# Kernel optimization log

Measured on AMD Instinct MI355X. Metric: run time of the kernel, lower is better.

The kernel has to match this reference:

```python
import jax, jax.numpy as jnp
import numpy as np

B, S, D_MODEL, NUM_HEADS, MAX_LEN = 4, 1024, 1024, 16, 1024
D_HEAD = D_MODEL // NUM_HEADS


def _skew(QEr):
    # QEr: (b, h, s, s). Music-Transformer skew: pad one col on the left,
    # reshape swapping the last two dims, drop the first row.
    b, h, r, c = QEr.shape
    padded = jnp.pad(QEr, ((0, 0), (0, 0), (0, 0), (1, 0)))  # (b,h,r,c+1)
    reshaped = padded.reshape(b, h, c + 1, r)
    return reshaped[:, :, 1:, :]  # (b,h,s,s)


def setup_inputs() -> dict:
    key = jax.random.key(0)
    ks = jax.random.split(key, 8)
    sc = 1.0 / np.sqrt(D_MODEL).astype(np.float32)
    return {
        "x": jax.random.normal(ks[0], (B, S, D_MODEL), jnp.float32),
        "Wq": jax.random.normal(ks[1], (D_MODEL, D_MODEL), jnp.float32) * sc,
        "bq": jnp.zeros((D_MODEL,), jnp.float32),
        "Wk": jax.random.normal(ks[2], (D_MODEL, D_MODEL), jnp.float32) * sc,
        "bk": jnp.zeros((D_MODEL,), jnp.float32),
        "Wv": jax.random.normal(ks[3], (D_MODEL, D_MODEL), jnp.float32) * sc,
        "bv": jnp.zeros((D_MODEL,), jnp.float32),
        "Er": jax.random.normal(ks[4], (MAX_LEN, D_HEAD), jnp.float32),
    }


def reference(x, Wq, bq, Wk, bk, Wv, bv, Er):
    b, s, _ = x.shape
    h, dh = NUM_HEADS, D_HEAD
    # projections -> (b, h, s, dh). Weights stored [in, out] (equiv. to torch W.T).
    q = (x @ Wq + bq).reshape(b, s, h, dh).transpose(0, 2, 1, 3)
    k = (x @ Wk + bk).reshape(b, s, h, dh).transpose(0, 2, 1, 3)
    v = (x @ Wv + bv).reshape(b, s, h, dh).transpose(0, 2, 1, 3)
    Er_t = Er[MAX_LEN - s:, :]                      # (s, dh)
    QEr = jnp.einsum('bhsd,td->bhst', q, Er_t)      # (b,h,s,s)
    Srel = _skew(QEr)
    scores = (jnp.einsum('bhsd,bhtd->bhst', q, k) + Srel) / np.float32(np.sqrt(dh))
    causal = jnp.tril(jnp.ones((s, s), bool))       # (s,s)
    scores = jnp.where(causal[None, None], scores, -jnp.inf)
    attn = jax.nn.softmax(scores, axis=-1)
    out = jnp.einsum('bhst,bhtd->bhsd', attn, v)    # (b,h,s,dh)
    return out.transpose(0, 2, 1, 3).reshape(b, s, h * dh)
```

## Files before the change

kernel.cpp:

```cpp
#include <hip/hip_runtime.h>
#include <hip/hip_bf16.h>
#include <math.h>

typedef __attribute__((ext_vector_type(8))) short short8;
typedef __attribute__((ext_vector_type(4))) float f32x4;
typedef __attribute__((ext_vector_type(4))) unsigned short us4;
typedef __attribute__((ext_vector_type(2))) unsigned int u32x2;

#define DM 1024
#define NH 16
#define DH 64
#define SS 1024
#define C2 0.180336879f

#define GLDS16(g, l) __builtin_amdgcn_global_load_lds(                      \
    (const __attribute__((address_space(1))) unsigned int*)(g),             \
    (__attribute__((address_space(3))) unsigned int*)(l), 16, 0, 0)

__device__ __forceinline__ unsigned short f2b(float f){
    unsigned int u = __float_as_uint(f);
    u += 0x7fffu + ((u >> 16) & 1u);
    return (unsigned short)(u >> 16);
}
__device__ __forceinline__ float b2f(unsigned short b){
    return __uint_as_float(((unsigned int)b) << 16);
}
__device__ __forceinline__ unsigned int cvt_pk_bf16(float lo, float hi){
    unsigned int r;
    asm volatile("v_cvt_pk_bf16_f32 %0, %1, %2" : "=v"(r) : "v"(lo), "v"(hi));
    return r;
}

__global__ __launch_bounds__(256) void cast_f32_bf16_k(const float* __restrict__ in,
                                                       unsigned short* __restrict__ out){
    int i = (blockIdx.x * 256 + threadIdx.x) * 4;
    float4 v = *(const float4*)(in + i);
    us4 o = { f2b(v.x), f2b(v.y), f2b(v.z), f2b(v.w) };
    *(us4*)(out + i) = o;
}

__global__ __launch_bounds__(256) void transpose_cast_w_k(const float* __restrict__ Wq,
                                                          const float* __restrict__ Wk,
                                                          const float* __restrict__ Wv,
                                                          unsigned short* __restrict__ wT){
    __shared__ float tile[32][33];
    const float* W = blockIdx.z==0 ? Wq : (blockIdx.z==1 ? Wk : Wv);
    int o0 = blockIdx.x*32, k0 = blockIdx.y*32;
    int tx = threadIdx.x, ty = threadIdx.y;
    #pragma unroll
    for (int i=0;i<32;i+=8) tile[ty+i][tx] = W[(k0+ty+i)*DM + o0+tx];
    __syncthreads();
    #pragma unroll
    for (int i=0;i<32;i+=8) wT[(blockIdx.z*DM + o0+ty+i)*DM + k0+tx] = f2b(tile[tx][ty+i]);
}

__global__ __launch_bounds__(256) void gemm_qkv_k(
    const unsigned short* __restrict__ xb, const unsigned short* __restrict__ wT,
    const float* __restrict__ bq, const float* __restrict__ bk, const float* __restrict__ bv,
    unsigned short* __restrict__ Qb, unsigned short* __restrict__ Kb, unsigned short* __restrict__ VTb)
{
    __shared__ unsigned short lda[128*32];
    __shared__ unsigned short ldb[128*32];
    const int tid = threadIdx.x;
    const int lane = tid & 63, w = tid >> 6;
    const int wr = w >> 1, wc = w & 1;
    const int lr = lane & 15, lk = (lane >> 4) * 8, lk4 = lane >> 4;
    const int m0 = blockIdx.y * 128, n0 = blockIdx.x * 128;
    const bool vblk = (n0 >= 2048);
    f32x4 acc[4][4] = {};
    for (int k0 = 0; k0 < DM; k0 += 32){
        #pragma unroll
        for (int p=0;p<2;p++){
            int idx = tid + p*256;
            int row = idx >> 2, cc = (idx & 3) * 8;
            GLDS16(&xb[(m0+row)*DM + k0 + cc], &lda[idx<<3]);
            GLDS16(&wT[(n0+row)*DM + k0 + cc], &ldb[idx<<3]);
        }
        __syncthreads();
        short8 a[4], b[4];
        #pragma unroll
        for (int m=0;m<4;m++) a[m] = *(const short8*)(&lda[(wr*64+m*16+lr)*32 + lk]);
        #pragma unroll
        for (int n=0;n<4;n++) b[n] = *(const short8*)(&ldb[(wc*64+n*16+lr)*32 + lk]);
        __builtin_amdgcn_s_setprio(1);
        if (vblk){
            #pragma unroll
            for (int m=0;m<4;m++)
                #pragma unroll
                for (int n=0;n<4;n++)
                    acc[m][n] = __builtin_amdgcn_mfma_f32_16x16x32_bf16(b[n], a[m], acc[m][n], 0,0,0);
        } else {
            #pragma unroll
            for (int m=0;m<4;m++)
                #pragma unroll
                for (int n=0;n<4;n++)
                    acc[m][n] = __builtin_amdgcn_mfma_f32_16x16x32_bf16(a[m], b[n], acc[m][n], 0,0,0);
        }
        __builtin_amdgcn_s_setprio(0);
        __syncthreads();
    }
    if (!vblk){
        #pragma unroll
        for (int m=0;m<4;m++){
            #pragma unroll
            for (int n=0;n<4;n++){
                int C = n0 + wc*64 + n*16 + lr;
                int proj = C >> 10, hd = C & 1023;
                float badd = (proj==0 ? bq : bk)[hd];
                int h = hd >> 6, d = hd & 63;
                #pragma unroll
                for (int r=0;r<4;r++){
                    int R = m0 + wr*64 + m*16 + lk4*4 + r;
                    int b_ = R >> 10, s = R & 1023;
                    float v = acc[m][n][r] + badd;
                    unsigned short val = f2b(proj==0 ? v*C2 : v);
                    (proj==0 ? Qb : Kb)[(((b_*NH)+h)*SS + s)*DH + d] = val;
                }
            }
        }
    } else {
        float badd[4][4];
        #pragma unroll
        for (int n=0;n<4;n++)
            #pragma unroll
            for (int r=0;r<4;r++)
                badd[n][r] = bv[n0-2048 + wc*64 + n*16 + lk4*4 + r];
        #pragma unroll
        for (int m=0;m<4;m++){
            int sb = m0 + wr*64 + m*16 + lr;
            int b_ = sb >> 10, sl = sb & 1023;
            #pragma unroll
            for (int n=0;n<4;n++){
                #pragma unroll
                for (int r=0;r<4;r++){
                    int hd = n0-2048 + wc*64 + n*16 + lk4*4 + r;
                    int h = hd >> 6, d = hd & 63;
                    VTb[(((b_*NH)+h)*DH + d)*SS + sl] = f2b(acc[m][n][r] + badd[n][r]);
                }
            }
        }
    }
}

__global__ __launch_bounds__(256) void attn_k(
    const unsigned short* __restrict__ Qb, const unsigned short* __restrict__ Kb,
    const unsigned short* __restrict__ VTb, const unsigned short* __restrict__ Erb,
    float* __restrict__ out)
{
    __shared__ unsigned short k_lds[64*64];
    __shared__ unsigned short vt_lds[64*64];
    __shared__ unsigned short er_lds[128*64];
    __shared__ unsigned short p_lds[64*64];
    __shared__ unsigned short rbt[4][80*20];

    const int tid = threadIdx.x, lane = tid & 63, w = tid >> 6;
    const int lr = lane & 15, lk4 = lane >> 4;
    const int bh = blockIdx.x;
    const int i0 = (int)(gridDim.y - 1 - blockIdx.y) * 64;
    const unsigned short* q_b  = Qb  + bh*SS*DH;
    const unsigned short* k_b  = Kb  + bh*SS*DH;
    const unsigned short* vt_b = VTb + bh*DH*SS;

    auto STAGE_K = [&](int j0){
        #pragma unroll
        for (int p=0;p<2;p++){
            int idx = tid + p*256;
            int row = idx >> 3, ch = idx & 7;
            GLDS16(&k_b[(j0+row)*DH + ((ch ^ (row&7))<<3)], &k_lds[idx<<3]);
        }
    };
    auto STAGE_VT = [&](int j0){
        #pragma unroll
        for (int p=0;p<2;p++){
            int idx = tid + p*256;
            int row = idx >> 3, ch = idx & 7;
            GLDS16(&vt_b[row*SS + j0 + ((ch ^ (row&7))<<3)], &vt_lds[idx<<3]);
        }
    };
    auto STAGE_ER = [&](int t0){
        #pragma unroll
        for (int p=0;p<4;p++){
            int idx = tid + p*256;
            int row = idx >> 3, ch = idx & 7;
            GLDS16(&Erb[(t0+row)*DH + ((ch ^ (row&7))<<3)], &er_lds[idx<<3]);
        }
    };

    const int ntiles = i0/64 + 1;
    STAGE_K(0);
    STAGE_ER(960 - i0);

    short8 qf[2];
    #pragma unroll
    for (int kk=0;kk<2;kk++)
        qf[kk] = *(const short8*)(&q_b[(i0 + w*16 + lr)*DH + kk*32 + lk4*8]);

    __syncthreads();

    f32x4 o_acc[4] = {};
    float l_r[4] = {0.f,0.f,0.f,0.f};
    unsigned short* rbw = &rbt[w][0];
    const int fbase = 3 - w;

    for (int t=0; t<ntiles; t++){
        const int j0 = t*64;
        STAGE_VT(j0);

        f32x4 s_acc[4] = {};
        f32x4 r_acc[5] = {};
        __builtin_amdgcn_s_setprio(1);
        #pragma unroll
        for (int kk=0;kk<2;kk++){
            const int sco = ((kk*4+lk4) ^ (lr&7)) << 3;
            #pragma unroll
            for (int n=0;n<4;n++){
                short8 kf = *(const short8*)(&k_lds[(n*16+lr)*64 + sco]);
                s_acc[n] = __builtin_amdgcn_mfma_f32_16x16x32_bf16(qf[kk], kf, s_acc[n], 0,0,0);
            }
            #pragma unroll
            for (int fi=0;fi<5;fi++){
                short8 ef = *(const short8*)(&er_lds[((fbase+fi)*16+lr)*64 + sco]);
                r_acc[fi] = __builtin_amdgcn_mfma_f32_16x16x32_bf16(qf[kk], ef, r_acc[fi], 0,0,0);
            }
        }
        __builtin_amdgcn_s_setprio(0);

        __syncthreads();
        if (t+1 < ntiles){
            STAGE_K(j0+64);
            STAGE_ER(960 - i0 + j0 + 64);
        }

        #pragma unroll
        for (int fi=0;fi<5;fi++){
            u32x2 pk;
            pk[0] = cvt_pk_bf16(r_acc[fi][0], r_acc[fi][1]);
            pk[1] = cvt_pk_bf16(r_acc[fi][2], r_acc[fi][3]);
            *(u32x2*)(&rbw[(fi*16+lr)*20 + lk4*4]) = pk;
        }

        float s2[4][4];
        #pragma unroll
        for (int r=0;r<4;r++){
            const int rr = lk4*4 + r;
            const int gb = (15 - rr + lr)*20 + rr;
            #pragma unroll
            for (int n=0;n<4;n++)
                s2[n][r] = s_acc[n][r] + b2f(rbw[gb + n*320]);
        }
        if (t == ntiles-1){
            #pragma unroll
            for (int r=0;r<4;r++){
                const int gi = i0 + w*16 + lk4*4 + r;
                #pragma unroll
                for (int n=0;n<4;n++)
                    if (j0 + n*16 + lr > gi) s2[n][r] = -INFINITY;
            }
        }
        #pragma unroll
        for (int r=0;r<4;r++){
            float p0 = __builtin_amdgcn_exp2f(s2[0][r]);
            float p1 = __builtin_amdgcn_exp2f(s2[1][r]);
            float p2 = __builtin_amdgcn_exp2f(s2[2][r]);
            float p3 = __builtin_amdgcn_exp2f(s2[3][r]);
            l_r[r] += (p0+p1)+(p2+p3);
            unsigned int u01 = cvt_pk_bf16(p0, p1);
            unsigned int u23 = cvt_pk_bf16(p2, p3);
            const int li = w*16 + lk4*4 + r;
            const int ro = li*64 + (lr&7);
            p_lds[ro + (((0 + (lr>>3)) ^ (li&7))<<3)] = (unsigned short)u01;
            p_lds[ro + (((2 + (lr>>3)) ^ (li&7))<<3)] = (unsigned short)(u01>>16);
            p_lds[ro + (((4 + (lr>>3)) ^ (li&7))<<3)] = (unsigned short)u23;
            p_lds[ro + (((6 + (lr>>3)) ^ (li&7))<<3)] = (unsigned short)(u23>>16);
        }

        __builtin_amdgcn_s_setprio(1);
        #pragma unroll
        for (int kk=0;kk<2;kk++){
            const int sco = ((kk*4+lk4) ^ (lr&7)) << 3;
            short8 pf = *(const short8*)(&p_lds[(w*16+lr)*64 + sco]);
            #pragma unroll
            for (int n=0;n<4;n++){
                short8 vf = *(const short8*)(&vt_lds[(n*16+lr)*64 + sco]);
                o_acc[n] = __builtin_amdgcn_mfma_f32_16x16x32_bf16(pf, vf, o_acc[n], 0,0,0);
            }
        }
        __builtin_amdgcn_s_setprio(0);
        __syncthreads();
    }

    #pragma unroll
    for (int r=0;r<4;r++){
        float l = l_r[r];
        #pragma unroll
        for (int msk=1; msk<16; msk<<=1) l += __shfl_xor(l, msk);
        l_r[r] = 1.0f / l;
    }
    const int b_ = bh >> 4, h = bh & 15;
    #pragma unroll
    for (int n=0;n<4;n++)
        #pragma unroll
        for (int r=0;r<4;r++){
            int li = w*16 + lk4*4 + r;
            int d = n*16 + lr;
            out[(b_*SS + i0 + li)*DM + h*DH + d] = o_acc[n][r] * l_r[r];
        }
}

extern "C" void kernel_launch(void* const* d_in, const int* in_sizes, int n_in,
                              void* d_out, int out_size, void* d_ws, size_t ws_size,
                              hipStream_t stream)
{
    const float* x  = (const float*)d_in[0];
    const float* Wq = (const float*)d_in[1];
    const float* bq = (const float*)d_in[2];
    const float* Wk = (const float*)d_in[3];
    const float* bk = (const float*)d_in[4];
    const float* Wv = (const float*)d_in[5];
    const float* bv = (const float*)d_in[6];
    const float* Er = (const float*)d_in[7];
    float* out = (float*)d_out;
    char* ws = (char*)d_ws;
    unsigned short* xb  = (unsigned short*)(ws);
    unsigned short* wT  = (unsigned short*)(ws + 8388608);
    unsigned short* erb = (unsigned short*)(ws + 14680064);
    unsigned short* Qb  = (unsigned short*)(ws + 14827520);
    unsigned short* Kb  = (unsigned short*)(ws + 23216128);
    unsigned short* VTb = (unsigned short*)(ws + 31604736);

    cast_f32_bf16_k<<<4096, 256, 0, stream>>>(x, xb);
    cast_f32_bf16_k<<<64, 256, 0, stream>>>(Er, erb);
    hipMemsetAsync(erb + 1024*DH, 0, 128*DH*sizeof(unsigned short), stream);
    transpose_cast_w_k<<<dim3(32,32,3), dim3(32,8), 0, stream>>>(Wq, Wk, Wv, wT);
    gemm_qkv_k<<<dim3(24,32), 256, 0, stream>>>(xb, wT, bq, bk, bv, Qb, Kb, VTb);
    attn_k<<<dim3(64,16), 256, 0, stream>>>(Qb, Kb, VTb, erb, out);
}
```

Baseline: 109.9 us.

## Deepen GEMM K-tile with swizzled LDS, stage V^T stores, pair causal attention tiles

The QKV GEMM now loads 64-wide K tiles with an XOR-swizzled LDS layout, halving the loop iterations and barriers. The V output is first transposed through shared memory so it can be written to VTb with coalesced 16-byte stores instead of scattered 2-byte writes. The attention kernel launches half as many blocks, and each block handles a short query tile paired with its long mirror (pr and 15-pr), which balances the causal work across blocks. The trade-offs are more LDS per GEMM block and fewer attention blocks in flight.

```diff
diff --git a/kernel.cpp b/kernel.cpp
--- a/kernel.cpp
+++ b/kernel.cpp
@@ -59,47 +59,43 @@
     const float* __restrict__ bq, const float* __restrict__ bk, const float* __restrict__ bv,
     unsigned short* __restrict__ Qb, unsigned short* __restrict__ Kb, unsigned short* __restrict__ VTb)
 {
-    __shared__ unsigned short lda[128*32];
-    __shared__ unsigned short ldb[128*32];
+    __shared__ unsigned short smem[2*128*64];
+    unsigned short* lda = smem;
+    unsigned short* ldb = smem + 128*64;
     const int tid = threadIdx.x;
     const int lane = tid & 63, w = tid >> 6;
     const int wr = w >> 1, wc = w & 1;
-    const int lr = lane & 15, lk = (lane >> 4) * 8, lk4 = lane >> 4;
+    const int lr = lane & 15, lk4 = lane >> 4;
     const int m0 = blockIdx.y * 128, n0 = blockIdx.x * 128;
-    const bool vblk = (n0 >= 2048);
     f32x4 acc[4][4] = {};
-    for (int k0 = 0; k0 < DM; k0 += 32){
-        #pragma unroll
-        for (int p=0;p<2;p++){
+    for (int k0 = 0; k0 < DM; k0 += 64){
+        #pragma unroll
+        for (int p=0;p<4;p++){
             int idx = tid + p*256;
-            int row = idx >> 2, cc = (idx & 3) * 8;
-            GLDS16(&xb[(m0+row)*DM + k0 + cc], &lda[idx<<3]);
-            GLDS16(&wT[(n0+row)*DM + k0 + cc], &ldb[idx<<3]);
+            int row = idx >> 3, ch = idx & 7;
+            GLDS16(&xb[(m0+row)*DM + k0 + ((ch ^ (row&7))<<3)], &lda[idx<<3]);
+            GLDS16(&wT[(n0+row)*DM + k0 + ((ch ^ (row&7))<<3)], &ldb[idx<<3]);
         }
         __syncthreads();
-        short8 a[4], b[4];
-        #pragma unroll
-        for (int m=0;m<4;m++) a[m] = *(const short8*)(&lda[(wr*64+m*16+lr)*32 + lk]);
-        #pragma unroll
-        for (int n=0;n<4;n++) b[n] = *(const short8*)(&ldb[(wc*64+n*16+lr)*32 + lk]);
-        __builtin_amdgcn_s_setprio(1);
-        if (vblk){
-            #pragma unroll
-            for (int m=0;m<4;m++)
-                #pragma unroll
-                for (int n=0;n<4;n++)
-                    acc[m][n] = __builtin_amdgcn_mfma_f32_16x16x32_bf16(b[n], a[m], acc[m][n], 0,0,0);
-        } else {
+        #pragma unroll
+        for (int kk=0;kk<2;kk++){
+            const int sco = ((kk*4+lk4) ^ (lr&7)) << 3;
+            short8 a[4], b[4];
+            #pragma unroll
+            for (int m=0;m<4;m++) a[m] = *(const short8*)(&lda[(wr*64+m*16+lr)*64 + sco]);
+            #pragma unroll
+            for (int n=0;n<4;n++) b[n] = *(const short8*)(&ldb[(wc*64+n*16+lr)*64 + sco]);
+            __builtin_amdgcn_s_setprio(1);
             #pragma unroll
             for (int m=0;m<4;m++)
                 #pragma unroll
                 for (int n=0;n<4;n++)
                     acc[m][n] = __builtin_amdgcn_mfma_f32_16x16x32_bf16(a[m], b[n], acc[m][n], 0,0,0);
-        }
-        __builtin_amdgcn_s_setprio(0);
+            __builtin_amdgcn_s_setprio(0);
+        }
         __syncthreads();
     }
-    if (!vblk){
+    if (n0 < 2048){
         #pragma unroll
         for (int m=0;m<4;m++){
             #pragma unroll
@@ -113,31 +109,36 @@
                     int R = m0 + wr*64 + m*16 + lk4*4 + r;
                     int b_ = R >> 10, s = R & 1023;
                     float v = acc[m][n][r] + badd;
-                    unsigned short val = f2b(proj==0 ? v*C2 : v);
-                    (proj==0 ? Qb : Kb)[(((b_*NH)+h)*SS + s)*DH + d] = val;
+                    (proj==0 ? Qb : Kb)[(((b_*NH)+h)*SS + s)*DH + d] = f2b(proj==0 ? v*C2 : v);
                 }
             }
         }
     } else {
-        float badd[4][4];
-        #pragma unroll
-        for (int n=0;n<4;n++)
-            #pragma unroll
-            for (int r=0;r<4;r++)
-                badd[n][r] = bv[n0-2048 + wc*64 + n*16 + lk4*4 + r];
-        #pragma unroll
-        for (int m=0;m<4;m++){
-            int sb = m0 + wr*64 + m*16 + lr;
-            int b_ = sb >> 10, sl = sb & 1023;
-            #pragma unroll
-            for (int n=0;n<4;n++){
-                #pragma unroll
-                for (int r=0;r<4;r++){
-                    int hd = n0-2048 + wc*64 + n*16 + lk4*4 + r;
-                    int h = hd >> 6, d = hd & 63;
-                    VTb[(((b_*NH)+h)*DH + d)*SS + sl] = f2b(acc[m][n][r] + badd[n][r]);
-                }
-            }
+        char* tb = (char*)smem;
+        #pragma unroll
+        for (int n=0;n<4;n++){
+            int Cl = wc*64 + n*16 + lr;
+            float badd = bv[n0 - 2048 + Cl];
+            #pragma unroll
+            for (int m=0;m<4;m++){
+                int R0 = wr*64 + m*16 + lk4*4;
+                us4 pk = { f2b(acc[m][n][0] + badd), f2b(acc[m][n][1] + badd),
+                           f2b(acc[m][n][2] + badd), f2b(acc[m][n][3] + badd) };
+                *(us4*)(tb + (Cl<<8) + (((R0<<1)) ^ ((Cl&7)<<4))) = pk;
+            }
+        }
+        __syncthreads();
+        const int b_ = m0 >> 10;
+        const int sres = m0 & 1023;
+        #pragma unroll
+        for (int q=0;q<8;q++){
+            int idx = q*256 + tid;
+            int dl = idx >> 4;
+            int sc = idx & 15;
+            short8 o = *(const short8*)(tb + (dl<<8) + (((sc<<4)) ^ ((dl&7)<<4)));
+            int Cg = n0 - 2048 + dl;
+            int h = Cg >> 6, d = Cg & 63;
+            *(short8*)(&VTb[(((b_*NH)+h)*DH + d)*SS + sres + sc*8]) = o;
         }
     }
 }
@@ -156,7 +157,7 @@
     const int tid = threadIdx.x, lane = tid & 63, w = tid >> 6;
     const int lr = lane & 15, lk4 = lane >> 4;
     const int bh = blockIdx.x;
-    const int i0 = (int)(gridDim.y - 1 - blockIdx.y) * 64;
+    const int pr = blockIdx.y;
     const unsigned short* q_b  = Qb  + bh*SS*DH;
     const unsigned short* k_b  = Kb  + bh*SS*DH;
     const unsigned short* vt_b = VTb + bh*DH*SS;
@@ -186,125 +187,131 @@
         }
     };
 
-    const int ntiles = i0/64 + 1;
-    STAGE_K(0);
-    STAGE_ER(960 - i0);
-
-    short8 qf[2];
-    #pragma unroll
-    for (int kk=0;kk<2;kk++)
-        qf[kk] = *(const short8*)(&q_b[(i0 + w*16 + lr)*DH + kk*32 + lk4*8]);
-
-    __syncthreads();
-
-    f32x4 o_acc[4] = {};
-    float l_r[4] = {0.f,0.f,0.f,0.f};
     unsigned short* rbw = &rbt[w][0];
     const int fbase = 3 - w;
 
-    for (int t=0; t<ntiles; t++){
-        const int j0 = t*64;
-        STAGE_VT(j0);
-
-        f32x4 s_acc[4] = {};
-        f32x4 r_acc[5] = {};
-        __builtin_amdgcn_s_setprio(1);
-        #pragma unroll
-        for (int kk=0;kk<2;kk++){
-            const int sco = ((kk*4+lk4) ^ (lr&7)) << 3;
-            #pragma unroll
-            for (int n=0;n<4;n++){
-                short8 kf = *(const short8*)(&k_lds[(n*16+lr)*64 + sco]);
-                s_acc[n] = __builtin_amdgcn_mfma_f32_16x16x32_bf16(qf[kk], kf, s_acc[n], 0,0,0);
-            }
+    for (int seg=0; seg<2; ++seg){
+        const int ib = seg ? 15 - pr : pr;
+        const int i0 = ib * 64;
+        const int ntiles = ib + 1;
+
+        STAGE_K(0);
+        STAGE_ER(960 - i0);
+
+        short8 qf[2];
+        #pragma unroll
+        for (int kk=0;kk<2;kk++)
+            qf[kk] = *(const short8*)(&q_b[(i0 + w*16 + lr)*DH + kk*32 + lk4*8]);
+
+        __syncthreads();
+
+        f32x4 o_acc[4] = {};
+        float l_r[4] = {0.f,0.f,0.f,0.f};
+
+        for (int t=0; t<ntiles; t++){
+            const int j0 = t*64;
+            STAGE_VT(j0);
+
+            f32x4 s_acc[4] = {};
+            f32x4 r_acc[5] = {};
+            __builtin_amdgcn_s_setprio(1);
+            #pragma unroll
+            for (int kk=0;kk<2;kk++){
+                const int sco = ((kk*4+lk4) ^ (lr&7)) << 3;
+                #pragma unroll
+                for (int n=0;n<4;n++){
+                    short8 kf = *(const short8*)(&k_lds[(n*16+lr)*64 + sco]);
+                    s_acc[n] = __builtin_amdgcn_mfma_f32_16x16x32_bf16(qf[kk], kf, s_acc[n], 0,0,0);
+                }
+                #pragma unroll
+                for (int fi=0;fi<5;fi++){
+                    short8 ef = *(const short8*)(&er_lds[((fbase+fi)*16+lr)*64 + sco]);
+                    r_acc[fi] = __builtin_amdgcn_mfma_f32_16x16x32_bf16(qf[kk], ef, r_acc[fi], 0,0,0);
+                }
+            }
+            __builtin_amdgcn_s_setprio(0);
+
+            __syncthreads();
+            if (t+1 < ntiles){
+                STAGE_K(j0+64);
+                STAGE_ER(960 - i0 + j0 + 64);
+            }
+
             #pragma unroll
             for (int fi=0;fi<5;fi++){
-                short8 ef = *(const short8*)(&er_lds[((fbase+fi)*16+lr)*64 + sco]);
-                r_acc[fi] = __builtin_amdgcn_mfma_f32_16x16x32_bf16(qf[kk], ef, r_acc[fi], 0,0,0);
-            }
-        }
-        __builtin_amdgcn_s_setprio(0);
-
-        __syncthreads();
-        if (t+1 < ntiles){
-            STAGE_K(j0+64);
-            STAGE_ER(960 - i0 + j0 + 64);
-        }
-
-        #pragma unroll
-        for (int fi=0;fi<5;fi++){
-            u32x2 pk;
-            pk[0] = cvt_pk_bf16(r_acc[fi][0], r_acc[fi][1]);
-            pk[1] = cvt_pk_bf16(r_acc[fi][2], r_acc[fi][3]);
-            *(u32x2*)(&rbw[(fi*16+lr)*20 + lk4*4]) = pk;
-        }
-
-        float s2[4][4];
+                u32x2 pk;
+                pk[0] = cvt_pk_bf16(r_acc[fi][0], r_acc[fi][1]);
+                pk[1] = cvt_pk_bf16(r_acc[fi][2], r_acc[fi][3]);
+                *(u32x2*)(&rbw[(fi*16+lr)*20 + lk4*4]) = pk;
+            }
+
+            float s2[4][4];
+            #pragma unroll
+            for (int r=0;r<4;r++){
+                const int rr = lk4*4 + r;
+                const int gb = (15 - rr + lr)*20 + rr;
+                #pragma unroll
+                for (int n=0;n<4;n++)
+                    s2[n][r] = s_acc[n][r] + b2f(rbw[gb + n*320]);
+            }
+            if (t == ntiles-1){
+                #pragma unroll
+                for (int r=0;r<4;r++){
+                    const int gi = i0 + w*16 + lk4*4 + r;
+                    #pragma unroll
+                    for (int n=0;n<4;n++)
+                        if (j0 + n*16 + lr > gi) s2[n][r] = -INFINITY;
+                }
+            }
+            #pragma unroll
+            for (int r=0;r<4;r++){
+                float p0 = __builtin_amdgcn_exp2f(s2[0][r]);
+                float p1 = __builtin_amdgcn_exp2f(s2[1][r]);
+                float p2 = __builtin_amdgcn_exp2f(s2[2][r]);
+                float p3 = __builtin_amdgcn_exp2f(s2[3][r]);
+                l_r[r] += (p0+p1)+(p2+p3);
+                unsigned int u01 = cvt_pk_bf16(p0, p1);
+                unsigned int u23 = cvt_pk_bf16(p2, p3);
+                const int li = w*16 + lk4*4 + r;
+                const int ro = li*64 + (lr&7);
+                p_lds[ro + (((0 + (lr>>3)) ^ (li&7))<<3)] = (unsigned short)u01;
+                p_lds[ro + (((2 + (lr>>3)) ^ (li&7))<<3)] = (unsigned short)(u01>>16);
+                p_lds[ro + (((4 + (lr>>3)) ^ (li&7))<<3)] = (unsigned short)u23;
+                p_lds[ro + (((6 + (lr>>3)) ^ (li&7))<<3)] = (unsigned short)(u23>>16);
+            }
+
+            __builtin_amdgcn_s_setprio(1);
+            #pragma unroll
+            for (int kk=0;kk<2;kk++){
+                const int sco = ((kk*4+lk4) ^ (lr&7)) << 3;
+                short8 pf = *(const short8*)(&p_lds[(w*16+lr)*64 + sco]);
+                #pragma unroll
+                for (int n=0;n<4;n++){
+                    short8 vf = *(const short8*)(&vt_lds[(n*16+lr)*64 + sco]);
+                    o_acc[n] = __builtin_amdgcn_mfma_f32_16x16x32_bf16(pf, vf, o_acc[n], 0,0,0);
+                }
+            }
+            __builtin_amdgcn_s_setprio(0);
+            __syncthreads();
+        }
+
         #pragma unroll
         for (int r=0;r<4;r++){
-            const int rr = lk4*4 + r;
-            const int gb = (15 - rr + lr)*20 + rr;
-            #pragma unroll
-            for (int n=0;n<4;n++)
-                s2[n][r] = s_acc[n][r] + b2f(rbw[gb + n*320]);
-        }
-        if (t == ntiles-1){
+            float l = l_r[r];
+            #pragma unroll
+            for (int msk=1; msk<16; msk<<=1) l += __shfl_xor(l, msk);
+            l_r[r] = 1.0f / l;
+        }
+        const int b_ = bh >> 4, h = bh & 15;
+        #pragma unroll
+        for (int n=0;n<4;n++)
             #pragma unroll
             for (int r=0;r<4;r++){
-                const int gi = i0 + w*16 + lk4*4 + r;
-                #pragma unroll
-                for (int n=0;n<4;n++)
-                    if (j0 + n*16 + lr > gi) s2[n][r] = -INFINITY;
-            }
-        }
-        #pragma unroll
-        for (int r=0;r<4;r++){
-            float p0 = __builtin_amdgcn_exp2f(s2[0][r]);
-            float p1 = __builtin_amdgcn_exp2f(s2[1][r]);
-            float p2 = __builtin_amdgcn_exp2f(s2[2][r]);
-            float p3 = __builtin_amdgcn_exp2f(s2[3][r]);
-            l_r[r] += (p0+p1)+(p2+p3);
-            unsigned int u01 = cvt_pk_bf16(p0, p1);
-            unsigned int u23 = cvt_pk_bf16(p2, p3);
-            const int li = w*16 + lk4*4 + r;
-            const int ro = li*64 + (lr&7);
-            p_lds[ro + (((0 + (lr>>3)) ^ (li&7))<<3)] = (unsigned short)u01;
-            p_lds[ro + (((2 + (lr>>3)) ^ (li&7))<<3)] = (unsigned short)(u01>>16);
-            p_lds[ro + (((4 + (lr>>3)) ^ (li&7))<<3)] = (unsigned short)u23;
-            p_lds[ro + (((6 + (lr>>3)) ^ (li&7))<<3)] = (unsigned short)(u23>>16);
-        }
-
-        __builtin_amdgcn_s_setprio(1);
-        #pragma unroll
-        for (int kk=0;kk<2;kk++){
-            const int sco = ((kk*4+lk4) ^ (lr&7)) << 3;
-            short8 pf = *(const short8*)(&p_lds[(w*16+lr)*64 + sco]);
-            #pragma unroll
-            for (int n=0;n<4;n++){
-                short8 vf = *(const short8*)(&vt_lds[(n*16+lr)*64 + sco]);
-                o_acc[n] = __builtin_amdgcn_mfma_f32_16x16x32_bf16(pf, vf, o_acc[n], 0,0,0);
-            }
-        }
-        __builtin_amdgcn_s_setprio(0);
-        __syncthreads();
+                int li = w*16 + lk4*4 + r;
+                int d = n*16 + lr;
+                out[(b_*SS + i0 + li)*DM + h*DH + d] = o_acc[n][r] * l_r[r];
+            }
     }
-
-    #pragma unroll
-    for (int r=0;r<4;r++){
-        float l = l_r[r];
-        #pragma unroll
-        for (int msk=1; msk<16; msk<<=1) l += __shfl_xor(l, msk);
-        l_r[r] = 1.0f / l;
-    }
-    const int b_ = bh >> 4, h = bh & 15;
-    #pragma unroll
-    for (int n=0;n<4;n++)
-        #pragma unroll
-        for (int r=0;r<4;r++){
-            int li = w*16 + lk4*4 + r;
-            int d = n*16 + lr;
-            out[(b_*SS + i0 + li)*DM + h*DH + d] = o_acc[n][r] * l_r[r];
-        }
 }
 
 extern "C" void kernel_launch(void* const* d_in, const int* in_sizes, int n_in,
@@ -333,5 +340,5 @@
     hipMemsetAsync(erb + 1024*DH, 0, 128*DH*sizeof(unsigned short), stream);
     transpose_cast_w_k<<<dim3(32,32,3), dim3(32,8), 0, stream>>>(Wq, Wk, Wv, wT);
     gemm_qkv_k<<<dim3(24,32), 256, 0, stream>>>(xb, wT, bq, bk, bv, Qb, Kb, VTb);
-    attn_k<<<dim3(64,16), 256, 0, stream>>>(Qb, Kb, VTb, erb, out);
-}
+    attn_k<<<dim3(64,8), 256, 0, stream>>>(Qb, Kb, VTb, erb, out);
+}
```

Result: faster. 93.51 us (-14.9%).
